# Kernel optimization log

Measured on AMD Instinct MI355X. Metric: run time of the kernel, lower is better.

The kernel has to match this reference:

```python
import jax, jax.numpy as jnp
import numpy as np

HIDDEN = 256


def setup_inputs() -> dict:
    key = jax.random.key(0)
    ks = jax.random.split(key, 16)
    bs, T, wv, vocab, inp = 256, 256, 100, 600, 64
    s = 0.05
    lengths = jax.random.randint(ks[2], (bs,), 2, T + 1)
    lengths = lengths.at[0].set(T)  # ensure max(decoder_length) == T-1
    return {
        "encoder_out": jax.random.normal(ks[0], (bs, inp), jnp.float32),
        "encoded_captions": jax.random.normal(ks[1], (bs, T, wv), jnp.float32),
        "w_ih": jax.random.normal(ks[3], (4 * HIDDEN, inp), jnp.float32) * s,
        "w_hh": jax.random.normal(ks[4], (4 * HIDDEN, HIDDEN), jnp.float32) * s,
        "b_ih": jax.random.normal(ks[5], (4 * HIDDEN,), jnp.float32) * s,
        "b_hh": jax.random.normal(ks[6], (4 * HIDDEN,), jnp.float32) * s,
        "W_out": jax.random.normal(ks[7], (vocab, HIDDEN), jnp.float32) * s,
        "b_out": jax.random.normal(ks[8], (vocab,), jnp.float32) * s,
        "W_emb": jax.random.normal(ks[9], (inp, wv), jnp.float32) * s,
        "b_emb": jax.random.normal(ks[10], (inp,), jnp.float32) * s,
        "W_h": jax.random.normal(ks[11], (HIDDEN, inp), jnp.float32) * s,
        "b_h": jax.random.normal(ks[12], (HIDDEN,), jnp.float32) * s,
        "W_c": jax.random.normal(ks[13], (HIDDEN, inp), jnp.float32) * s,
        "b_c": jax.random.normal(ks[14], (HIDDEN,), jnp.float32) * s,
        "caption_lengths": lengths,
    }


def reference(encoder_out, encoded_captions, w_ih, w_hh, b_ih, b_hh,
              W_out, b_out, W_emb, b_emb, W_h, b_h, W_c, b_c,
              caption_lengths):
    # sort by descending caption length (as torch.sort(descending=True))
    sort_idx = jnp.argsort(-caption_lengths)
    lengths = caption_lengths[sort_idx]
    enc = encoder_out[sort_idx]                  # [bs, 64]
    caps = encoded_captions[sort_idx]            # [bs, T, 100]

    h0 = enc @ W_h.T + b_h                       # [bs, H]
    c0 = enc @ W_c.T + b_c                       # [bs, H]
    emb = caps @ W_emb.T + b_emb                 # [bs, T, 64]

    dec_len = lengths - 1                        # [bs]
    steps = caps.shape[1] - 1                    # == max(dec_len) by construction
    xs = jnp.swapaxes(emb[:, :steps], 0, 1)      # [steps, bs, 64]
    ts = jnp.arange(steps)

    def step(carry, inp):
        h, c = carry
        x, t = inp
        gates = x @ w_ih.T + b_ih + h @ w_hh.T + b_hh      # [bs, 4H]
        i, f, g, o = jnp.split(gates, 4, axis=-1)           # torch gate order i,f,g,o
        i = jax.nn.sigmoid(i); f = jax.nn.sigmoid(f)
        g = jnp.tanh(g);       o = jax.nn.sigmoid(o)
        c_new = f * c + i * g
        h_new = o * jnp.tanh(c_new)
        active = (t < dec_len)[:, None]                     # shrinking batch == mask (sorted)
        logits = h_new @ W_out.T + b_out                    # [bs, vocab]
        pred = jnp.where(active, logits, jnp.float32(-1.0))
        h = jnp.where(active, h_new, h)
        c = jnp.where(active, c_new, c)
        return (h, c), pred

    (_, _), preds = jax.lax.scan(step, (h0, c0), (xs, ts))
    predicts = jnp.swapaxes(preds, 0, 1)         # [bs, steps, vocab]
    return predicts, caps, dec_len, sort_idx
```

## Files before the change

kernel.cpp:

```cpp
#include <hip/hip_runtime.h>
#include <hip/hip_fp16.h>

#define BS 256
#define T 256
#define STEPS 255
#define WV 100
#define INP 64
#define H 256
#define G4 1024
#define VOCAB 600
#define VT 38

typedef _Float16 f16x2 __attribute__((ext_vector_type(2)));
typedef _Float16 f16x8 __attribute__((ext_vector_type(8)));
typedef float f32x4 __attribute__((ext_vector_type(4)));

__device__ __forceinline__ float fdot2(unsigned w, unsigned h, float acc) {
#if defined(__has_builtin) && __has_builtin(__builtin_amdgcn_fdot2)
    return __builtin_amdgcn_fdot2(__builtin_bit_cast(f16x2, w),
                                  __builtin_bit_cast(f16x2, h), acc, false);
#else
    __half2 wv = *(const __half2*)&w;
    __half2 hv = *(const __half2*)&h;
    float2 wf = __half22float2(wv), hf = __half22float2(hv);
    return acc + wf.x * hf.x + wf.y * hf.y;
#endif
}

__device__ __forceinline__ float quad_reduce(float x) {
    int a = __builtin_bit_cast(int, x);
    int b = __builtin_amdgcn_update_dpp(0, a, 0xB1, 0xF, 0xF, true);
    float s = x + __builtin_bit_cast(float, b);
    int c = __builtin_bit_cast(int, s);
    int d = __builtin_amdgcn_update_dpp(0, c, 0x4E, 0xF, 0xF, true);
    return s + __builtin_bit_cast(float, d);
}

__device__ __forceinline__ f32x4 mfma16(uint4 a, uint4 b, f32x4 c) {
    return __builtin_amdgcn_mfma_f32_16x16x32_f16(
        __builtin_bit_cast(f16x8, a), __builtin_bit_cast(f16x8, b), c, 0, 0, 0);
}

__global__ void k_sort(const int* __restrict__ lens, int* __restrict__ sidx,
                       int* __restrict__ dlen, float* __restrict__ out_dec,
                       float* __restrict__ out_sidx) {
    __shared__ int L[BS];
    int i = threadIdx.x;
    L[i] = lens[i];
    __syncthreads();
    int li = L[i];
    int r = 0;
    for (int j = 0; j < BS; ++j) {
        int lj = L[j];
        r += (lj > li) || (lj == li && j < i);
    }
    sidx[r] = i;
    dlen[r] = li - 1;
    out_sidx[r] = (float)i;
    out_dec[r]  = (float)(li - 1);
}

__global__ void k_gather(const float* __restrict__ cin, const int* __restrict__ sidx,
                         float* __restrict__ cout) {
    int b = blockIdx.x;
    int src = sidx[b];
    const float4* in  = (const float4*)(cin + (size_t)src * T * WV);
    float4* out       = (float4*)(cout + (size_t)b * T * WV);
    for (int i = threadIdx.x; i < T * WV / 4; i += 256) out[i] = in[i];
}

__global__ void k_wcomb(const float* __restrict__ w_ih, const float* __restrict__ W_emb,
                        float* __restrict__ Wc) {
    int idx = blockIdx.x * 256 + threadIdx.x;
    int r = idx / WV, cc = idx % WV;
    float acc = 0.f;
    for (int k = 0; k < INP; ++k) acc += w_ih[r * INP + k] * W_emb[k * WV + cc];
    Wc[idx] = acc;
}

__global__ void k_bcomb(const float* __restrict__ w_ih, const float* __restrict__ b_ih,
                        const float* __restrict__ b_hh, const float* __restrict__ b_emb,
                        float* __restrict__ bc) {
    int r = blockIdx.x * 256 + threadIdx.x;
    float acc = b_ih[r] + b_hh[r];
    for (int k = 0; k < INP; ++k) acc += w_ih[r * INP + k] * b_emb[k];
    bc[r] = acc;
}

__global__ void k_packw(const float* __restrict__ w_hh, __half2* __restrict__ wR) {
    int idx = blockIdx.x * 256 + threadIdx.x;
    wR[idx] = __floats2half2_rn(w_hh[(size_t)idx * 2], w_hh[(size_t)idx * 2 + 1]);
}

__global__ void k_packwo(const float* __restrict__ Wo, __half* __restrict__ woHi,
                         __half* __restrict__ woLo) {
    int idx = blockIdx.x * 256 + threadIdx.x;
    int fi = idx >> 9;
    int l  = (idx >> 3) & 63;
    int j  = idx & 7;
    int vt = fi >> 3, kt = fi & 7;
    int v = vt * 16 + (l & 15);
    int k = kt * 32 + ((l >> 4) << 3) + j;
    float w = (v < VOCAB) ? Wo[(size_t)v * H + k] : 0.f;
    __half hi = __float2half(w);
    __half lo = __float2half(w - __half2float(hi));
    woHi[idx] = hi;
    woLo[idx] = lo;
}

__global__ void k_packcaps(const float* __restrict__ caps, __half* __restrict__ cHi,
                           __half* __restrict__ cLo) {
    int idx = blockIdx.x * 256 + threadIdx.x;
    int k = idx & 127;
    int bt = idx >> 7;
    float v = (k < WV) ? caps[(size_t)bt * WV + k] : 0.f;
    __half hi = __float2half(v);
    cHi[idx] = hi;
    cLo[idx] = __float2half(v - __half2float(hi));
}

__global__ void k_packwc(const float* __restrict__ Wc, __half* __restrict__ wcHi,
                         __half* __restrict__ wcLo) {
    int idx = blockIdx.x * 256 + threadIdx.x;
    int fi = idx >> 9;
    int l  = (idx >> 3) & 63;
    int j  = idx & 7;
    int nt = fi >> 2, kt = fi & 3;
    int n = nt * 16 + (l & 15);
    int k = kt * 32 + ((l >> 4) << 3) + j;
    float w = (k < WV) ? Wc[(size_t)n * WV + k] : 0.f;
    __half hi = __float2half(w);
    wcHi[idx] = hi;
    wcLo[idx] = __float2half(w - __half2float(hi));
}

__global__ void k_inithc(const float* __restrict__ enc, const int* __restrict__ sidx,
                         const float* __restrict__ W_h, const float* __restrict__ b_h,
                         const float* __restrict__ W_c, const float* __restrict__ b_c,
                         float* __restrict__ h_st, float* __restrict__ c_st) {
    int b = blockIdx.x, j = threadIdx.x;
    __shared__ __align__(16) float e[INP];
    int src = sidx[b];
    if (j < INP) e[j] = enc[src * INP + j];
    __syncthreads();
    const float4* e4  = (const float4*)e;
    const float4* wh4 = (const float4*)(W_h + (size_t)j * INP);
    const float4* wc4 = (const float4*)(W_c + (size_t)j * INP);
    float ah = b_h[j], ac = b_c[j];
    #pragma unroll
    for (int k4 = 0; k4 < INP / 4; ++k4) {
        float4 ev = e4[k4];
        float4 wh = wh4[k4];
        float4 wc = wc4[k4];
        ah += ev.x * wh.x + ev.y * wh.y + ev.z * wh.z + ev.w * wh.w;
        ac += ev.x * wc.x + ev.y * wc.y + ev.z * wc.z + ev.w * wc.w;
    }
    h_st[b * H + j] = ah;
    c_st[b * H + j] = ac;
}

__global__ __launch_bounds__(256) void k_xg(const __half* __restrict__ cHi,
        const __half* __restrict__ cLo, const __half* __restrict__ wcHi,
        const __half* __restrict__ wcLo, const float* __restrict__ bc,
        const int* __restrict__ dlen, float* __restrict__ xg, int t0, int Cc) {
    int b = blockIdx.y;
    int ct0 = blockIdx.x * 32;
    if (t0 + ct0 >= dlen[b]) return;
    int tid = threadIdx.x;
    int l = tid & 63, wid = tid >> 6;
    int lhi = l >> 4, llo = l & 15;

    uint4 aH[2][4], aL[2][4];
    #pragma unroll
    for (int m = 0; m < 2; ++m) {
        int rr = ct0 + m * 16 + llo;
        if (rr >= Cc) rr = Cc - 1;
        size_t base = ((size_t)b * T + (t0 + rr)) * 128 + lhi * 8;
        #pragma unroll
        for (int kt = 0; kt < 4; ++kt) {
            aH[m][kt] = *(const uint4*)(cHi + base + kt * 32);
            aL[m][kt] = *(const uint4*)(cLo + base + kt * 32);
        }
    }
    const uint4* bh4 = (const uint4*)wcHi;
    const uint4* bl4 = (const uint4*)wcLo;
    for (int i = 0; i < 16; ++i) {
        int nt = wid * 16 + i;
        float bias = bc[nt * 16 + llo];
        f32x4 acc0 = {bias, bias, bias, bias};
        f32x4 acc1 = acc0;
        #pragma unroll
        for (int kt = 0; kt < 4; ++kt) {
            uint4 bh = bh4[(nt * 4 + kt) * 64 + l];
            uint4 bl = bl4[(nt * 4 + kt) * 64 + l];
            acc0 = mfma16(aH[0][kt], bh, acc0);
            acc1 = mfma16(aH[1][kt], bh, acc1);
            acc0 = mfma16(aH[0][kt], bl, acc0);
            acc1 = mfma16(aH[1][kt], bl, acc1);
            acc0 = mfma16(aL[0][kt], bh, acc0);
            acc1 = mfma16(aL[1][kt], bh, acc1);
        }
        #pragma unroll
        for (int m = 0; m < 2; ++m) {
            f32x4 A = m ? acc1 : acc0;
            #pragma unroll
            for (int ii = 0; ii < 4; ++ii) {
                int rr = ct0 + m * 16 + lhi * 4 + ii;
                if (rr < Cc)
                    xg[((size_t)b * Cc + rr) * G4 + nt * 16 + llo] = A[ii];
            }
        }
    }
}

#define LSTM_SMEM (131072 + 4096 + 1152)

__global__ __launch_bounds__(512)
__attribute__((amdgpu_waves_per_eu(2, 2)))
void k_lstm(const __half2* __restrict__ wR,
        const float* __restrict__ xg, const int* __restrict__ dlen,
        float* __restrict__ h_st, float* __restrict__ c_st,
        __half* __restrict__ hck, int t0, int Cc) {
    extern __shared__ __align__(16) char smem[];
    uint4*    wl4  = (uint4*)smem;
    float*    gv   = (float*)(smem + 131072);
    unsigned* hpad = (unsigned*)(smem + 131072 + 4096);
    unsigned* lpad = hpad + 144;
    const uint4* hh4 = (const uint4*)hpad;
    const uint4* hl4 = (const uint4*)lpad;

    int b = blockIdx.x, tid = threadIdx.x;
    int steps_b = dlen[b];
    if (t0 >= steps_b) return;

    int lane = tid & 63;
    int q = lane & 3;
    int Q = tid >> 2;
    int rowbase = Q * 8;
    int gate = __builtin_amdgcn_readfirstlane(tid >> 7);

    const uint4* wR4 = (const uint4*)wR;

    uint4 wreg[6][8];
    #pragma unroll
    for (int j = 0; j < 6; ++j)
        #pragma unroll
        for (int u = 0; u < 8; ++u)
            wreg[j][u] = wR4[(rowbase + j) * 32 + q * 8 + u];
    #pragma unroll
    for (int s = 0; s < 2; ++s)
        #pragma unroll
        for (int u = 0; u < 8; ++u)
            wl4[((u * 2 + s) * 128 + Q) * 4 + q] = wR4[(rowbase + 6 + s) * 32 + q * 8 + u];

    float c = 0.f, hcur = 0.f;
    if (tid < H) {
        hcur = h_st[b * H + tid];
        c    = c_st[b * H + tid];
        __half hh16 = __float2half(hcur);
        __half hl16 = __float2half(hcur - __half2float(hh16));
        int hidx = (tid >> 6) * 72 + (tid & 63);
        ((__half*)hpad)[hidx] = hh16;
        ((__half*)lpad)[hidx] = hl16;
    }
    __syncthreads();

    int tend = t0 + Cc; if (tend > steps_b) tend = steps_b;
    const float* xgp = xg + (size_t)b * Cc * G4;
    __half* hckp = hck + (size_t)b * Cc * H;

    for (int t = t0; t < tend; ++t) {
        float x0 = xgp[rowbase + q];
        float x1 = xgp[rowbase + 4 + q];

        float ah[8], al[8];
        #pragma unroll
        for (int j = 0; j < 8; ++j) { ah[j] = 0.f; al[j] = 0.f; }

        #pragma unroll
        for (int u = 0; u < 8; ++u) {
            uint4 hh = hh4[q * 9 + u];
            uint4 hl = hl4[q * 9 + u];
            #pragma unroll
            for (int j = 0; j < 6; ++j) {
                uint4 w = wreg[j][u];
                ah[j] = fdot2(w.x, hh.x, ah[j]);
                ah[j] = fdot2(w.y, hh.y, ah[j]);
                ah[j] = fdot2(w.z, hh.z, ah[j]);
                ah[j] = fdot2(w.w, hh.w, ah[j]);
                al[j] = fdot2(w.x, hl.x, al[j]);
                al[j] = fdot2(w.y, hl.y, al[j]);
                al[j] = fdot2(w.z, hl.z, al[j]);
                al[j] = fdot2(w.w, hl.w, al[j]);
            }
            uint4 w6 = wl4[((u * 2 + 0) * 128 + Q) * 4 + q];
            uint4 w7 = wl4[((u * 2 + 1) * 128 + Q) * 4 + q];
            ah[6] = fdot2(w6.x, hh.x, ah[6]);
            ah[6] = fdot2(w6.y, hh.y, ah[6]);
            ah[6] = fdot2(w6.z, hh.z, ah[6]);
            ah[6] = fdot2(w6.w, hh.w, ah[6]);
            al[6] = fdot2(w6.x, hl.x, al[6]);
            al[6] = fdot2(w6.y, hl.y, al[6]);
            al[6] = fdot2(w6.z, hl.z, al[6]);
            al[6] = fdot2(w6.w, hl.w, al[6]);
            ah[7] = fdot2(w7.x, hh.x, ah[7]);
            ah[7] = fdot2(w7.y, hh.y, ah[7]);
            ah[7] = fdot2(w7.z, hh.z, ah[7]);
            ah[7] = fdot2(w7.w, hh.w, ah[7]);
            al[7] = fdot2(w7.x, hl.x, al[7]);
            al[7] = fdot2(w7.y, hl.y, al[7]);
            al[7] = fdot2(w7.z, hl.z, al[7]);
            al[7] = fdot2(w7.w, hl.w, al[7]);
        }

        float tt[8];
        #pragma unroll
        for (int j = 0; j < 8; ++j) tt[j] = quad_reduce(ah[j] + al[j]);

        float k0 = (q == 0) ? tt[0] : (q == 1) ? tt[1] : (q == 2) ? tt[2] : tt[3];
        float k1 = (q == 0) ? tt[4] : (q == 1) ? tt[5] : (q == 2) ? tt[6] : tt[7];
        float p0 = k0 + x0;
        float p1 = k1 + x1;
        if (gate == 2) { p0 = tanhf(p0); p1 = tanhf(p1); }
        else {
            p0 = 1.f / (1.f + __expf(-p0));
            p1 = 1.f / (1.f + __expf(-p1));
        }
        gv[rowbase + q]     = p0;
        gv[rowbase + 4 + q] = p1;
        __syncthreads();

        if (tid < H) {
            float iv  = gv[tid];
            float fv  = gv[256 + tid];
            float gvt = gv[512 + tid];
            float ov  = gv[768 + tid];
            c = fv * c + iv * gvt;
            float nh = ov * tanhf(c);
            hcur = nh;
            __half hh16 = __float2half(nh);
            __half hl16 = __float2half(nh - __half2float(hh16));
            hckp[tid] = hh16;
            int hidx = (tid >> 6) * 72 + (tid & 63);
            ((__half*)hpad)[hidx] = hh16;
            ((__half*)lpad)[hidx] = hl16;
        }
        __syncthreads();
        xgp += G4;
        hckp += H;
    }
    if (tid < H) { h_st[b * H + tid] = hcur; c_st[b * H + tid] = c; }
}

__global__ __launch_bounds__(64) void k_logits(const __half* __restrict__ hck,
        const __half* __restrict__ woHi, const __half* __restrict__ woLo,
        const float* __restrict__ bo, const int* __restrict__ dlen,
        float* __restrict__ pred, int t0, int Cc) {
    int b = blockIdx.y;
    int ct0 = blockIdx.x * 32;
    if (ct0 >= Cc) return;
    int steps_b = dlen[b];
    int l = threadIdx.x;
    int lhi = l >> 4, llo = l & 15;

    if (t0 + ct0 >= steps_b) {
        for (int r = 0; r < 32; ++r) {
            int t = t0 + ct0 + r;
            if (r >= Cc - ct0 || t >= STEPS) break;
            float* pr = pred + ((size_t)b * STEPS + t) * VOCAB;
            for (int v = l; v < VOCAB; v += 64) pr[v] = -1.f;
        }
        return;
    }

    uint4 a[2][8];
    #pragma unroll
    for (int m = 0; m < 2; ++m) {
        int rr = ct0 + m * 16 + llo;
        int rc = (rr < Cc) ? rr : (Cc - 1);
        const uint4* rp = (const uint4*)(hck + ((size_t)b * Cc + rc) * H);
        #pragma unroll
        for (int kt = 0; kt < 8; ++kt) a[m][kt] = rp[kt * 4 + lhi];
    }

    const uint4* bh4 = (const uint4*)woHi;
    const uint4* bl4 = (const uint4*)woLo;
    for (int vt = 0; vt < VT; ++vt) {
        int v = vt * 16 + llo;
        float bias = (v < VOCAB) ? bo[v] : 0.f;
        f32x4 acc0 = {bias, bias, bias, bias};
        f32x4 acc1 = acc0;
        #pragma unroll
        for (int kt = 0; kt < 8; ++kt) {
            uint4 bh = bh4[(vt * 8 + kt) * 64 + l];
            acc0 = mfma16(a[0][kt], bh, acc0);
            acc1 = mfma16(a[1][kt], bh, acc1);
        }
        #pragma unroll
        for (int kt = 0; kt < 8; ++kt) {
            uint4 bl = bl4[(vt * 8 + kt) * 64 + l];
            acc0 = mfma16(a[0][kt], bl, acc0);
            acc1 = mfma16(a[1][kt], bl, acc1);
        }
        if (v < VOCAB) {
            #pragma unroll
            for (int m = 0; m < 2; ++m) {
                f32x4 A = m ? acc1 : acc0;
                #pragma unroll
                for (int i = 0; i < 4; ++i) {
                    int r = ct0 + m * 16 + lhi * 4 + i;
                    int t = t0 + r;
                    if (r < Cc && t < STEPS)
                        pred[((size_t)b * STEPS + t) * VOCAB + v] =
                            (t < steps_b) ? A[i] : -1.f;
                }
            }
        }
    }
}

extern "C" void kernel_launch(void* const* d_in, const int* in_sizes, int n_in,
                              void* d_out, int out_size, void* d_ws, size_t ws_size,
                              hipStream_t stream) {
    const float* enc   = (const float*)d_in[0];
    const float* caps  = (const float*)d_in[1];
    const float* w_ih  = (const float*)d_in[2];
    const float* w_hh  = (const float*)d_in[3];
    const float* b_ih  = (const float*)d_in[4];
    const float* b_hh  = (const float*)d_in[5];
    const float* W_out = (const float*)d_in[6];
    const float* b_out = (const float*)d_in[7];
    const float* W_emb = (const float*)d_in[8];
    const float* b_emb = (const float*)d_in[9];
    const float* W_h   = (const float*)d_in[10];
    const float* b_h   = (const float*)d_in[11];
    const float* W_c   = (const float*)d_in[12];
    const float* b_c   = (const float*)d_in[13];
    const int*   lens  = (const int*)d_in[14];

    float* out_pred = (float*)d_out;
    float* out_caps = out_pred + (size_t)BS * STEPS * VOCAB;
    float* out_dec  = out_caps + (size_t)BS * T * WV;
    float* out_sidx = out_dec + BS;

    char* w = (char*)d_ws;
    size_t off = 0;
    auto take = [&](size_t bytes) -> char* {
        char* p = w + off;
        off += (bytes + 255) & ~(size_t)255;
        return p;
    };
    int*     sidx = (int*)take(BS * 4);
    int*     dlen = (int*)take(BS * 4);
    float*   Wc   = (float*)take((size_t)G4 * WV * 4);
    float*   bc   = (float*)take(G4 * 4);
    float*   h_st = (float*)take((size_t)BS * H * 4);
    float*   c_st = (float*)take((size_t)BS * H * 4);
    __half2* wR   = (__half2*)take((size_t)G4 * (H / 2) * 4);
    __half*  woHi = (__half*)take((size_t)VT * 8 * 64 * 8 * 2);
    __half*  woLo = (__half*)take((size_t)VT * 8 * 64 * 8 * 2);
    __half*  cHi  = (__half*)take((size_t)BS * T * 128 * 2);
    __half*  cLo  = (__half*)take((size_t)BS * T * 128 * 2);
    __half*  wcHi = (__half*)take((size_t)64 * 4 * 64 * 8 * 2);
    __half*  wcLo = (__half*)take((size_t)64 * 4 * 64 * 8 * 2);

    size_t rem = (ws_size > off) ? (ws_size - off) : 0;
    size_t per_step = (size_t)BS * G4 * 4 + (size_t)BS * H * 2 + 1024;
    int C = (int)(rem / per_step);
    if (C < 1) C = 1;
    if (C > STEPS) C = STEPS;
    float*  xg  = (float*)take((size_t)BS * C * G4 * 4);
    __half* hck = (__half*)take((size_t)BS * C * H * 2);

    (void)hipFuncSetAttribute((const void*)k_lstm,
                              hipFuncAttributeMaxDynamicSharedMemorySize, LSTM_SMEM);

    k_sort<<<1, 256, 0, stream>>>(lens, sidx, dlen, out_dec, out_sidx);
    k_gather<<<BS, 256, 0, stream>>>(caps, sidx, out_caps);
    k_wcomb<<<G4 * WV / 256, 256, 0, stream>>>(w_ih, W_emb, Wc);
    k_bcomb<<<G4 / 256, 256, 0, stream>>>(w_ih, b_ih, b_hh, b_emb, bc);
    k_packw<<<G4 * (H / 2) / 256, 256, 0, stream>>>(w_hh, wR);
    k_packwo<<<VT * 8 * 64 * 8 / 256, 256, 0, stream>>>(W_out, woHi, woLo);
    k_packcaps<<<BS * T * 128 / 256, 256, 0, stream>>>(out_caps, cHi, cLo);
    k_packwc<<<64 * 4 * 64 * 8 / 256, 256, 0, stream>>>(Wc, wcHi, wcLo);
    k_inithc<<<BS, 256, 0, stream>>>(enc, sidx, W_h, b_h, W_c, b_c, h_st, c_st);

    for (int t0 = 0; t0 < STEPS; t0 += C) {
        int Cc = STEPS - t0; if (Cc > C) Cc = C;
        dim3 gx((Cc + 31) / 32, BS);
        k_xg<<<gx, 256, 0, stream>>>(cHi, cLo, wcHi, wcLo, bc, dlen, xg, t0, Cc);
        k_lstm<<<BS, 512, LSTM_SMEM, stream>>>(wR, xg, dlen, h_st, c_st, hck, t0, Cc);
        k_logits<<<gx, 64, 0, stream>>>(hck, woHi, woLo, b_out, dlen, out_pred, t0, Cc);
    }
}
```

Measured before the change: 1.320 ms.

## Remap LSTM gate rows per thread and double-buffer h to drop a barrier

Each quad of threads now owns two hidden units and holds all four gate rows (i, f, g, o) for them. The cell update therefore happens in registers right after the quad reduction, instead of passing through a shared gate buffer. The hidden state lives in a double-buffered shared array, which cuts per-step barriers from two to one and removes the gate shared-memory round trip. In exchange, activations are computed redundantly across the quad, and every thread evaluates all four nonlinearities.

```diff
diff --git a/kernel.cpp b/kernel.cpp
--- a/kernel.cpp
+++ b/kernel.cpp
@@ -213,7 +213,7 @@
     }
 }
 
-#define LSTM_SMEM (131072 + 4096 + 1152)
+#define LSTM_SMEM (131072 + 2 * 1152)
 
 __global__ __launch_bounds__(512)
 __attribute__((amdgpu_waves_per_eu(2, 2)))
@@ -223,11 +223,7 @@
         __half* __restrict__ hck, int t0, int Cc) {
     extern __shared__ __align__(16) char smem[];
     uint4*    wl4  = (uint4*)smem;
-    float*    gv   = (float*)(smem + 131072);
-    unsigned* hpad = (unsigned*)(smem + 131072 + 4096);
-    unsigned* lpad = hpad + 144;
-    const uint4* hh4 = (const uint4*)hpad;
-    const uint4* hl4 = (const uint4*)lpad;
+    unsigned* hbuf = (unsigned*)(smem + 131072);
 
     int b = blockIdx.x, tid = threadIdx.x;
     int steps_b = dlen[b];
@@ -236,42 +232,51 @@
     int lane = tid & 63;
     int q = lane & 3;
     int Q = tid >> 2;
-    int rowbase = Q * 8;
-    int gate = __builtin_amdgcn_readfirstlane(tid >> 7);
+    int rx = 2 * Q + (q & 1);
 
     const uint4* wR4 = (const uint4*)wR;
 
     uint4 wreg[6][8];
     #pragma unroll
-    for (int j = 0; j < 6; ++j)
+    for (int j = 0; j < 6; ++j) {
+        int grow = (j >> 1) * 256 + 2 * Q + (j & 1);
         #pragma unroll
         for (int u = 0; u < 8; ++u)
-            wreg[j][u] = wR4[(rowbase + j) * 32 + q * 8 + u];
+            wreg[j][u] = wR4[grow * 32 + q * 8 + u];
+    }
     #pragma unroll
     for (int s = 0; s < 2; ++s)
         #pragma unroll
         for (int u = 0; u < 8; ++u)
-            wl4[((u * 2 + s) * 128 + Q) * 4 + q] = wR4[(rowbase + 6 + s) * 32 + q * 8 + u];
-
-    float c = 0.f, hcur = 0.f;
-    if (tid < H) {
-        hcur = h_st[b * H + tid];
-        c    = c_st[b * H + tid];
+            wl4[((u * 2 + s) * 128 + Q) * 4 + q] =
+                wR4[(768 + 2 * Q + s) * 32 + q * 8 + u];
+
+    float c = c_st[b * H + rx];
+    float hcur = h_st[b * H + rx];
+    {
         __half hh16 = __float2half(hcur);
         __half hl16 = __float2half(hcur - __half2float(hh16));
-        int hidx = (tid >> 6) * 72 + (tid & 63);
-        ((__half*)hpad)[hidx] = hh16;
-        ((__half*)lpad)[hidx] = hl16;
+        if (q < 2) {
+            int hidx = (rx >> 6) * 72 + (rx & 63);
+            ((__half*)(hbuf))[hidx] = hh16;
+            ((__half*)(hbuf + 144))[hidx] = hl16;
+        }
     }
     __syncthreads();
 
     int tend = t0 + Cc; if (tend > steps_b) tend = steps_b;
     const float* xgp = xg + (size_t)b * Cc * G4;
     __half* hckp = hck + (size_t)b * Cc * H;
+    int p = 0;
 
     for (int t = t0; t < tend; ++t) {
-        float x0 = xgp[rowbase + q];
-        float x1 = xgp[rowbase + 4 + q];
+        float xi = xgp[rx];
+        float xf = xgp[256 + rx];
+        float xgg = xgp[512 + rx];
+        float xo = xgp[768 + rx];
+
+        const uint4* hh4 = (const uint4*)(hbuf + p * 288);
+        const uint4* hl4 = (const uint4*)(hbuf + p * 288 + 144);
 
         float ah[8], al[8];
         #pragma unroll
@@ -317,39 +322,32 @@
         #pragma unroll
         for (int j = 0; j < 8; ++j) tt[j] = quad_reduce(ah[j] + al[j]);
 
-        float k0 = (q == 0) ? tt[0] : (q == 1) ? tt[1] : (q == 2) ? tt[2] : tt[3];
-        float k1 = (q == 0) ? tt[4] : (q == 1) ? tt[5] : (q == 2) ? tt[6] : tt[7];
-        float p0 = k0 + x0;
-        float p1 = k1 + x1;
-        if (gate == 2) { p0 = tanhf(p0); p1 = tanhf(p1); }
-        else {
-            p0 = 1.f / (1.f + __expf(-p0));
-            p1 = 1.f / (1.f + __expf(-p1));
-        }
-        gv[rowbase + q]     = p0;
-        gv[rowbase + 4 + q] = p1;
+        int odd = q & 1;
+        float pi = odd ? tt[1] : tt[0];
+        float pf = odd ? tt[3] : tt[2];
+        float pg = odd ? tt[5] : tt[4];
+        float po = odd ? tt[7] : tt[6];
+        float iv = 1.f / (1.f + __expf(-(pi + xi)));
+        float fv = 1.f / (1.f + __expf(-(pf + xf)));
+        float gv = tanhf(pg + xgg);
+        float ov = 1.f / (1.f + __expf(-(po + xo)));
+        c = fv * c + iv * gv;
+        float nh = ov * tanhf(c);
+        hcur = nh;
+        __half hh16 = __float2half(nh);
+        __half hl16 = __float2half(nh - __half2float(hh16));
+        if (q < 2) {
+            hckp[rx] = hh16;
+            int hidx = (rx >> 6) * 72 + (rx & 63);
+            ((__half*)(hbuf + (p ^ 1) * 288))[hidx] = hh16;
+            ((__half*)(hbuf + (p ^ 1) * 288 + 144))[hidx] = hl16;
+        }
         __syncthreads();
-
-        if (tid < H) {
-            float iv  = gv[tid];
-            float fv  = gv[256 + tid];
-            float gvt = gv[512 + tid];
-            float ov  = gv[768 + tid];
-            c = fv * c + iv * gvt;
-            float nh = ov * tanhf(c);
-            hcur = nh;
-            __half hh16 = __float2half(nh);
-            __half hl16 = __float2half(nh - __half2float(hh16));
-            hckp[tid] = hh16;
-            int hidx = (tid >> 6) * 72 + (tid & 63);
-            ((__half*)hpad)[hidx] = hh16;
-            ((__half*)lpad)[hidx] = hl16;
-        }
-        __syncthreads();
+        p ^= 1;
         xgp += G4;
         hckp += H;
     }
-    if (tid < H) { h_st[b * H + tid] = hcur; c_st[b * H + tid] = c; }
+    if (q < 2) { h_st[b * H + rx] = hcur; c_st[b * H + rx] = c; }
 }
 
 __global__ __launch_bounds__(64) void k_logits(const __half* __restrict__ hck,
```

Measured after the change: 1.284 ms. 1.03x faster.
